# Kernel tuning notes

Hardware: AMD Instinct MI355X
Metric: run time of the kernel (lower is better)

The kernel has to match this reference:

```python
import jax, jax.numpy as jnp
import numpy as np

V = 30000      # user_size / vocab
NINP = 64      # d_word_vec
H = 64         # d_inner_hid
D_NET = 64     # net embedding dim
POS_DIM = 8
NNL1 = 25
NNL2 = 10
MEM = 3
B = 32
LP1 = 101      # seq length before trimming last token


def setup_inputs() -> dict:
    key = jax.random.key(0)
    ks = jax.random.split(key, 16)
    L = LP1 - 1
    u = lambda k, sh: jax.random.uniform(k, sh, jnp.float32, -0.1, 0.1)
    return {
        "encoder_w": u(ks[0], (V, NINP)),
        "pos_w": u(ks[1], (1000, POS_DIM)),
        "w_ih": u(ks[2], (3 * H, NINP + POS_DIM)),
        "w_hh": u(ks[3], (3 * H, H)),
        "b_ih": jnp.zeros((3 * H,), jnp.float32),
        "b_hh": jnp.zeros((3 * H,), jnp.float32),
        "gcn1_w": u(ks[4], (H, H)),
        "gcn1_b": jnp.zeros((H,), jnp.float32),
        "gcn2_w": u(ks[5], (H, D_NET)),
        "gcn2_b": jnp.zeros((H,), jnp.float32),
        "dec_w": u(ks[6], (V, 2 * H)),
        "dec_b": jnp.zeros((V,), jnp.float32),
        "net_emb_tab": jax.random.normal(ks[7], (V, D_NET), jnp.float32),
        "seq": jax.random.randint(ks[8], (B, LP1), 0, V),
        "nb2": jax.random.randint(ks[9], (B * L * NNL1, NNL2), 0, V),
    }


def _forward(encoder_w, pos_w, w_ih, w_hh, b_ih, b_hh,
             gcn1_w, gcn1_b, gcn2_w, gcn2_b, dec_w, dec_b,
             net_emb_tab, seq, nb2):
    inp = seq[:, :-1]                      # (B, L)
    b, L = inp.shape

    # --- GraphSAGE-style 2-hop aggregation (dropout=0, eval mode) ---
    feats = net_emb_tab[nb2]               # (B*L*NNL1, NNL2, D_NET) irregular gather
    nf2 = jax.nn.relu(jnp.mean(feats @ gcn2_w.T + gcn2_b, axis=1))   # (B*L*NNL1, H)
    nf2 = nf2.reshape(b * L, NNL1, H)
    nf1 = jax.nn.relu(jnp.mean(nf2 @ gcn1_w.T + gcn1_b, axis=1))     # (B*L, H)
    nf1 = nf1.reshape(b, L, H)
    # causal memory window of size MEM=3 with zero left-padding, plain mean
    net_pad = jnp.concatenate([jnp.zeros((b, MEM - 1, H), nf1.dtype), nf1], axis=1)
    net_mem = (net_pad[:, 0:L] + net_pad[:, 1:L + 1] + net_pad[:, 2:L + 2]) / MEM  # (B,L,H)

    # --- embeddings + positional ---
    emb = encoder_w[inp]                   # (B, L, NINP)
    pos = jnp.broadcast_to(pos_w[:L][None], (b, L, POS_DIM))
    x = jnp.concatenate([emb, pos], axis=-1)   # (B, L, NINP+POS_DIM)

    # --- GRUCell recurrence via scan (torch gate order: r, z, n) ---
    def gru_step(h, xt):
        gi = xt @ w_ih.T + b_ih            # (B, 3H)
        gh = h @ w_hh.T + b_hh             # (B, 3H)
        i_r, i_z, i_n = jnp.split(gi, 3, axis=-1)
        h_r, h_z, h_n = jnp.split(gh, 3, axis=-1)
        r = jax.nn.sigmoid(i_r + h_r)
        z = jax.nn.sigmoid(i_z + h_z)
        n = jnp.tanh(i_n + r * h_n)
        h_new = (1.0 - z) * n + z * h
        return h_new, h_new

    h0 = jnp.zeros((b, H), x.dtype)
    hidden, hs = jax.lax.scan(gru_step, h0, x.transpose(1, 0, 2))  # hs: (L, B, H)

    outputs = jnp.concatenate([hs.transpose(1, 0, 2), net_mem], axis=-1)  # (B, L, 2H)
    decoded = outputs @ dec_w.T + dec_b    # (B, L, V)

    # --- previous-user scatter mask: -inf at seq[b, :t+1] and at index 0 ---
    tri = jnp.tril(jnp.ones((L, L), bool))
    idx = jnp.where(tri[None], inp[:, None, :], 0)                 # (B, L, L)
    idx = jnp.concatenate([idx, jnp.zeros((b, L, 1), idx.dtype)], axis=-1)
    bidx = jnp.arange(b)[:, None, None]
    tidx = jnp.arange(L)[None, :, None]
    mask = jnp.zeros((b, L, V), decoded.dtype).at[bidx, tidx, idx].set(-jnp.inf)

    result = (decoded + mask).reshape(b * L, V)
    return result, hidden


def reference(encoder_w, pos_w, w_ih, w_hh, b_ih, b_hh,
              gcn1_w, gcn1_b, gcn2_w, gcn2_b, dec_w, dec_b,
              net_emb_tab, seq, nb2):
    return _forward(encoder_w, pos_w, w_ih, w_hh, b_ih, b_hh,
                    gcn1_w, gcn1_b, gcn2_w, gcn2_b, dec_w, dec_b,
                    net_emb_tab, seq, nb2)
```

## Files before the change

### kernel.cpp

```cpp
#include <hip/hip_runtime.h>
#include <math.h>

#define SEQLEN 100
#define BATCH 32
#define HDIM 64
#define VOCAB 30000
#define KDIM 128

#define MASK_NEG (-1.0e30f)

typedef __attribute__((ext_vector_type(8))) short short8;
typedef __attribute__((ext_vector_type(4))) short short4v;
typedef __attribute__((ext_vector_type(4))) float f32x4;

#define WSB_GI     0
#define WSB_NF1    2457600
#define WSB_ABF    3276800
#define WSB_TABBF  4096000
#define WSB_DECWBF 7936000

__device__ __forceinline__ float sigmoidf_(float x) { return 1.0f / (1.0f + expf(-x)); }

__device__ __forceinline__ short f2bf(float f) {
    unsigned u = __builtin_bit_cast(unsigned, f);
    return (short)((u + 0x7fffu + ((u >> 16) & 1u)) >> 16);
}
__device__ __forceinline__ float bf2f(unsigned short s) {
    unsigned u = ((unsigned)s) << 16;
    return __builtin_bit_cast(float, u);
}

__global__ __launch_bounds__(256) void prep_kernel(
    const float* __restrict__ enc, const float* __restrict__ pos_w,
    const float* __restrict__ w_ih, const float* __restrict__ b_ih,
    const int* __restrict__ seq, const float* __restrict__ tab,
    const float* __restrict__ dec_w,
    float* __restrict__ gi, short* __restrict__ tabbf, short* __restrict__ decwbf)
{
    const int tid = threadIdx.x;
    if (blockIdx.x < 100) {
        __shared__ float Wih[192 * 73];
        for (int j = tid; j < 13824; j += 256) {
            int r = j / 72, k = j - r * 72;
            Wih[r * 73 + k] = w_ih[j];
        }
        __syncthreads();
        const int t = blockIdx.x;
        if (tid < 192) {
            const int r = tid;
            const float* wr = &Wih[r * 73];
            const float* pr = pos_w + t * 8;
            float poss = b_ih[r];
            #pragma unroll
            for (int k = 0; k < 8; ++k) poss += pr[k] * wr[64 + k];
            for (int b = 0; b < 32; ++b) {
                const int token = seq[b * 101 + t];
                const float* er = enc + (size_t)token * 64;
                float p0 = 0.f, p1 = 0.f, p2 = 0.f, p3 = 0.f;
                #pragma unroll
                for (int k = 0; k < 64; k += 4) {
                    p0 += er[k + 0] * wr[k + 0];
                    p1 += er[k + 1] * wr[k + 1];
                    p2 += er[k + 2] * wr[k + 2];
                    p3 += er[k + 3] * wr[k + 3];
                }
                gi[(size_t)(t * 32 + b) * 192 + r] = poss + ((p0 + p1) + (p2 + p3));
            }
        }
    } else {
        for (int j = (blockIdx.x - 100) * 256 + tid; j < 1440000; j += 380 * 256) {
            if (j < 480000) {
                float4 v = reinterpret_cast<const float4*>(tab)[j];
                short4v o;
                o[0] = f2bf(v.x); o[1] = f2bf(v.y); o[2] = f2bf(v.z); o[3] = f2bf(v.w);
                *reinterpret_cast<short4v*>(&tabbf[(size_t)j * 4]) = o;
            } else {
                const int k = j - 480000;
                float4 v = reinterpret_cast<const float4*>(dec_w)[k];
                short4v o;
                o[0] = f2bf(v.x); o[1] = f2bf(v.y); o[2] = f2bf(v.z); o[3] = f2bf(v.w);
                *reinterpret_cast<short4v*>(&decwbf[(size_t)k * 4]) = o;
            }
        }
    }
}

union SM {
    struct { float W2t[64][64]; float W1t[64][64]; float sbuf[4][64]; } g;
    struct { float h[64]; float gh[192]; } r;
};
__global__ __launch_bounds__(256) void gcn_gru_kernel(
    const short* __restrict__ tabbf, const int* __restrict__ nb2,
    const float* __restrict__ gcn1_w, const float* __restrict__ gcn1_b,
    const float* __restrict__ gcn2_w, const float* __restrict__ gcn2_b,
    float* __restrict__ nf1,
    const float* __restrict__ gi, const float* __restrict__ w_hh,
    const float* __restrict__ b_hh, short* __restrict__ Abf,
    float* __restrict__ hid_out)
{
    __shared__ SM sm;
    const int tid = threadIdx.x;

    if (blockIdx.x < 32) {
        const int b = blockIdx.x;
        const int r = tid;
        float wreg[64];
        float bh = 0.0f;
        if (r < 192) {
            #pragma unroll
            for (int q = 0; q < 16; ++q) {
                float4 v = *reinterpret_cast<const float4*>(w_hh + r * 64 + q * 4);
                wreg[q * 4 + 0] = v.x; wreg[q * 4 + 1] = v.y;
                wreg[q * 4 + 2] = v.z; wreg[q * 4 + 3] = v.w;
            }
            bh = b_hh[r];
        }
        if (r < 64) sm.r.h[r] = 0.0f;
        __syncthreads();

        for (int t = 0; t < SEQLEN; ++t) {
            if (r < 192) {
                float p0 = bh, p1 = 0.f, p2 = 0.f, p3 = 0.f;
                #pragma unroll
                for (int d = 0; d < 64; d += 4) {
                    const float4 hv = *reinterpret_cast<const float4*>(&sm.r.h[d]);
                    p0 += hv.x * wreg[d + 0];
                    p1 += hv.y * wreg[d + 1];
                    p2 += hv.z * wreg[d + 2];
                    p3 += hv.w * wreg[d + 3];
                }
                sm.r.gh[r] = (p0 + p1) + (p2 + p3);
            }
            __syncthreads();
            if (r < 64) {
                const float* gib = gi + (size_t)(t * 32 + b) * 192;
                float rg = sigmoidf_(gib[r] + sm.r.gh[r]);
                float zg = sigmoidf_(gib[64 + r] + sm.r.gh[64 + r]);
                float ng = tanhf(gib[128 + r] + rg * sm.r.gh[128 + r]);
                float hn = (1.0f - zg) * ng + zg * sm.r.h[r];
                sm.r.h[r] = hn;
                Abf[(size_t)(b * SEQLEN + t) * KDIM + r] = f2bf(hn);
                if (t == SEQLEN - 1) hid_out[b * 64 + r] = hn;
            }
            __syncthreads();
        }
        return;
    }

    for (int idx = tid; idx < 4096; idx += 256) {
        int e = idx >> 6, d = idx & 63;
        sm.g.W2t[d][e] = gcn2_w[idx];
        sm.g.W1t[d][e] = gcn1_w[idx];
    }
    __syncthreads();

    const int wave = tid >> 6;
    const int lane = tid & 63;
    const int p = (blockIdx.x - 32) * 4 + wave;
    const float b2 = gcn2_b[lane];
    const int* __restrict__ nbb = nb2 + (size_t)p * 250;

    float acc = 0.0f;
    for (int i = 0; i < 25; ++i) {
        const int* nb = nbb + i * 10;
        float s0 = 0.f, s1 = 0.f;
        #pragma unroll
        for (int j = 0; j < 10; j += 2) {
            s0 += bf2f((unsigned short)tabbf[(size_t)nb[j] * 64 + lane]);
            s1 += bf2f((unsigned short)tabbf[(size_t)nb[j + 1] * 64 + lane]);
        }
        sm.g.sbuf[wave][lane] = (s0 + s1) * 0.1f;
        __syncthreads();
        float p0 = 0.f, p1 = 0.f, p2 = 0.f, p3 = 0.f;
        #pragma unroll
        for (int d = 0; d < 64; d += 4) {
            p0 += sm.g.sbuf[wave][d + 0] * sm.g.W2t[d + 0][lane];
            p1 += sm.g.sbuf[wave][d + 1] * sm.g.W2t[d + 1][lane];
            p2 += sm.g.sbuf[wave][d + 2] * sm.g.W2t[d + 2][lane];
            p3 += sm.g.sbuf[wave][d + 3] * sm.g.W2t[d + 3][lane];
        }
        acc += fmaxf(((p0 + p1) + (p2 + p3)) + b2, 0.0f);
        __syncthreads();
    }

    sm.g.sbuf[wave][lane] = acc * (1.0f / 25.0f);
    __syncthreads();
    float p0 = 0.f, p1 = 0.f, p2 = 0.f, p3 = 0.f;
    #pragma unroll
    for (int d = 0; d < 64; d += 4) {
        p0 += sm.g.sbuf[wave][d + 0] * sm.g.W1t[d + 0][lane];
        p1 += sm.g.sbuf[wave][d + 1] * sm.g.W1t[d + 1][lane];
        p2 += sm.g.sbuf[wave][d + 2] * sm.g.W1t[d + 2][lane];
        p3 += sm.g.sbuf[wave][d + 3] * sm.g.W1t[d + 3][lane];
    }
    nf1[p * 64 + lane] = fmaxf(((p0 + p1) + (p2 + p3)) + gcn1_b[lane], 0.0f);
}

__global__ __launch_bounds__(256) void netmem_kernel(const float* __restrict__ nf1, short* __restrict__ Abf)
{
    const int idx = blockIdx.x * 256 + threadIdx.x;
    if (idx >= 3200 * 64) return;
    const int p = idx >> 6, e = idx & 63;
    const int t = p % SEQLEN;
    float v = nf1[idx];
    if (t >= 1) v += nf1[idx - 64];
    if (t >= 2) v += nf1[idx - 128];
    Abf[(size_t)p * KDIM + 64 + e] = f2bf(v * (1.0f / 3.0f));
}

#define DN_PANELS 118
#define DM_BLKS   25
#define DNBLK (DM_BLKS * DN_PANELS)
__global__ __launch_bounds__(512) void decode_mfma(
    const short* __restrict__ Abf, const short* __restrict__ Bwbf,
    const float* __restrict__ bias, float* __restrict__ C)
{
    const int lid = blockIdx.x;
    const int q = DNBLK >> 3, r = DNBLK & 7;
    const int xcd = lid & 7, idx = lid >> 3;
    const int swz = (xcd < r ? xcd * (q + 1) : r * (q + 1) + (xcd - r) * q) + idx;
    const int mblk = swz / DN_PANELS;
    const int npanel = swz - mblk * DN_PANELS;

    const int tid = threadIdx.x;
    const int wid = tid >> 6, lane = tid & 63;
    const int lrow = lane & 15;
    const int lkg = lane >> 4;
    const int m0 = mblk * 128 + (wid >> 2) * 64;
    const int n0 = npanel * 256 + (wid & 3) * 64;

    f32x4 acc[4][4];
    #pragma unroll
    for (int mi = 0; mi < 4; ++mi)
        #pragma unroll
        for (int ni = 0; ni < 4; ++ni) acc[mi][ni] = (f32x4)0.0f;

    #pragma unroll
    for (int kc = 0; kc < 4; ++kc) {
        const int kof = kc * 32 + lkg * 8;
        short8 a[4], b[4];
        #pragma unroll
        for (int mi = 0; mi < 4; ++mi)
            a[mi] = *reinterpret_cast<const short8*>(Abf + (size_t)(m0 + mi * 16 + lrow) * KDIM + kof);
        #pragma unroll
        for (int ni = 0; ni < 4; ++ni) {
            const int row = n0 + ni * 16 + lrow;
            b[ni] = (row < VOCAB)
                ? *reinterpret_cast<const short8*>(Bwbf + (size_t)row * KDIM + kof)
                : (short8)0;
        }
        #pragma unroll
        for (int mi = 0; mi < 4; ++mi)
            #pragma unroll
            for (int ni = 0; ni < 4; ++ni)
                acc[mi][ni] = __builtin_amdgcn_mfma_f32_16x16x32_bf16(b[ni], a[mi], acc[mi][ni], 0, 0, 0);
    }

    int colb[4];
    f32x4 bias4[4];
    #pragma unroll
    for (int ni = 0; ni < 4; ++ni) {
        colb[ni] = n0 + ni * 16 + lkg * 4;
        bias4[ni] = (colb[ni] < VOCAB) ? *reinterpret_cast<const f32x4*>(&bias[colb[ni]]) : (f32x4)0.0f;
    }
    #pragma unroll
    for (int mi = 0; mi < 4; ++mi) {
        const size_t rowoff = (size_t)(m0 + mi * 16 + lrow) * VOCAB;
        #pragma unroll
        for (int ni = 0; ni < 4; ++ni) {
            if (colb[ni] < VOCAB)
                *reinterpret_cast<f32x4*>(&C[rowoff + colb[ni]]) = acc[mi][ni] + bias4[ni];
        }
    }
}

__global__ __launch_bounds__(256) void mask_kernel(const int* __restrict__ seq, float* __restrict__ out)
{
    const int w = blockIdx.x * 4 + (threadIdx.x >> 6);
    const int lane = threadIdx.x & 63;
    const int b = w / SEQLEN, t = w % SEQLEN;
    float* row = out + (size_t)w * VOCAB;
    if (lane == 0) row[0] = MASK_NEG;
    for (int j = lane; j <= t; j += 64) row[seq[b * 101 + j]] = MASK_NEG;
}

extern "C" void kernel_launch(void* const* d_in, const int* in_sizes, int n_in,
                              void* d_out, int out_size, void* d_ws, size_t ws_size,
                              hipStream_t stream) {
    const float* encoder_w = (const float*)d_in[0];
    const float* pos_w     = (const float*)d_in[1];
    const float* w_ih      = (const float*)d_in[2];
    const float* w_hh      = (const float*)d_in[3];
    const float* b_ih      = (const float*)d_in[4];
    const float* b_hh      = (const float*)d_in[5];
    const float* gcn1_w    = (const float*)d_in[6];
    const float* gcn1_b    = (const float*)d_in[7];
    const float* gcn2_w    = (const float*)d_in[8];
    const float* gcn2_b    = (const float*)d_in[9];
    const float* dec_w     = (const float*)d_in[10];
    const float* dec_b     = (const float*)d_in[11];
    const float* net_tab   = (const float*)d_in[12];
    const int*   seq       = (const int*)d_in[13];
    const int*   nb2       = (const int*)d_in[14];

    float* out = (float*)d_out;
    float* hid_out = out + (size_t)3200 * VOCAB;

    char* ws = (char*)d_ws;
    float* gi     = (float*)(ws + WSB_GI);
    float* nf1    = (float*)(ws + WSB_NF1);
    short* Abf    = (short*)(ws + WSB_ABF);
    short* tabbf  = (short*)(ws + WSB_TABBF);
    short* decwbf = (short*)(ws + WSB_DECWBF);

    prep_kernel<<<dim3(480), dim3(256), 0, stream>>>(encoder_w, pos_w, w_ih, b_ih, seq, net_tab, dec_w,
                                                     gi, tabbf, decwbf);
    gcn_gru_kernel<<<dim3(832), dim3(256), 0, stream>>>(tabbf, nb2, gcn1_w, gcn1_b, gcn2_w, gcn2_b,
                                                        nf1, gi, w_hh, b_hh, Abf, hid_out);
    netmem_kernel<<<dim3(800), dim3(256), 0, stream>>>(nf1, Abf);
    decode_mfma<<<dim3(DNBLK), dim3(512), 0, stream>>>(Abf, decwbf, dec_b, out);
    mask_kernel<<<dim3(800), dim3(256), 0, stream>>>(seq, out);
}
```

Baseline: 310.1 us.

## Fuse previous-user mask into decode GEMM epilogue and retile to 64-row blocks

```diff
diff --git a/kernel.cpp b/kernel.cpp
--- a/kernel.cpp
+++ b/kernel.cpp
@@ -208,26 +208,34 @@
     Abf[(size_t)p * KDIM + 64 + e] = f2bf(v * (1.0f / 3.0f));
 }
 
+#define DM_BLKS   50
 #define DN_PANELS 118
-#define DM_BLKS   25
 #define DNBLK (DM_BLKS * DN_PANELS)
-__global__ __launch_bounds__(512) void decode_mfma(
+__global__ __launch_bounds__(256, 3) void decode_mfma(
     const short* __restrict__ Abf, const short* __restrict__ Bwbf,
-    const float* __restrict__ bias, float* __restrict__ C)
+    const float* __restrict__ bias, const int* __restrict__ seq,
+    float* __restrict__ C)
 {
     const int lid = blockIdx.x;
     const int q = DNBLK >> 3, r = DNBLK & 7;
     const int xcd = lid & 7, idx = lid >> 3;
     const int swz = (xcd < r ? xcd * (q + 1) : r * (q + 1) + (xcd - r) * q) + idx;
-    const int mblk = swz / DN_PANELS;
-    const int npanel = swz - mblk * DN_PANELS;
+    const int npanel = swz / DM_BLKS;
+    const int mblk = swz - npanel * DM_BLKS;
 
     const int tid = threadIdx.x;
     const int wid = tid >> 6, lane = tid & 63;
     const int lrow = lane & 15;
     const int lkg = lane >> 4;
-    const int m0 = mblk * 128 + (wid >> 2) * 64;
-    const int n0 = npanel * 256 + (wid & 3) * 64;
+    const int m0 = mblk * 64;
+    const int N0 = npanel * 256;
+    const int n0 = N0 + wid * 64;
+
+    __shared__ int seq_l[200];
+    const int b0 = m0 / SEQLEN;
+    const int b1 = (m0 + 63) / SEQLEN;
+    if (tid < 100) seq_l[tid] = seq[b0 * 101 + tid];
+    else if (tid < 200 && b1 != b0) seq_l[tid] = seq[b1 * 101 + (tid - 100)];
 
     f32x4 acc[4][4];
     #pragma unroll
@@ -272,16 +280,20 @@
                 *reinterpret_cast<f32x4*>(&C[rowoff + colb[ni]]) = acc[mi][ni] + bias4[ni];
         }
     }
-}
-
-__global__ __launch_bounds__(256) void mask_kernel(const int* __restrict__ seq, float* __restrict__ out)
-{
-    const int w = blockIdx.x * 4 + (threadIdx.x >> 6);
-    const int lane = threadIdx.x & 63;
-    const int b = w / SEQLEN, t = w % SEQLEN;
-    float* row = out + (size_t)w * VOCAB;
-    if (lane == 0) row[0] = MASK_NEG;
-    for (int j = lane; j <= t; j += 64) row[seq[b * 101 + j]] = MASK_NEG;
+
+    __syncthreads();
+    if (tid < 64) {
+        const int row = m0 + tid;
+        const int b = row / SEQLEN;
+        const int t = row - b * SEQLEN;
+        const int* sl = seq_l + (b - b0) * 100;
+        float* crow = C + (size_t)row * VOCAB;
+        if (N0 == 0) crow[0] = MASK_NEG;
+        for (int j = 0; j <= t; ++j) {
+            const int tok = sl[j];
+            if (tok >= N0 && tok < N0 + 256) crow[tok] = MASK_NEG;
+        }
+    }
 }
 
 extern "C" void kernel_launch(void* const* d_in, const int* in_sizes, int n_in,
@@ -318,6 +330,5 @@
     gcn_gru_kernel<<<dim3(832), dim3(256), 0, stream>>>(tabbf, nb2, gcn1_w, gcn1_b, gcn2_w, gcn2_b,
                                                         nf1, gi, w_hh, b_hh, Abf, hid_out);
     netmem_kernel<<<dim3(800), dim3(256), 0, stream>>>(nf1, Abf);
-    decode_mfma<<<dim3(DNBLK), dim3(512), 0, stream>>>(Abf, decwbf, dec_b, out);
-    mask_kernel<<<dim3(800), dim3(256), 0, stream>>>(seq, out);
-}
+    decode_mfma<<<dim3(DNBLK), dim3(256), 0, stream>>>(Abf, decwbf, dec_b, seq, out);
+}
```

After: 316.9 us. 2.2% more time.

## Fuse kernels: gather fp32 GCN directly, merge netmem into GRU, mask in decode epilogue

Applied to the files above, without the earlier changes.

```diff
diff --git a/kernel.cpp b/kernel.cpp
--- a/kernel.cpp
+++ b/kernel.cpp
@@ -16,8 +16,7 @@
 #define WSB_GI     0
 #define WSB_NF1    2457600
 #define WSB_ABF    3276800
-#define WSB_TABBF  4096000
-#define WSB_DECWBF 7936000
+#define WSB_DECWBF 4096000
 
 __device__ __forceinline__ float sigmoidf_(float x) { return 1.0f / (1.0f + expf(-x)); }
 
@@ -25,30 +24,80 @@
     unsigned u = __builtin_bit_cast(unsigned, f);
     return (short)((u + 0x7fffu + ((u >> 16) & 1u)) >> 16);
 }
-__device__ __forceinline__ float bf2f(unsigned short s) {
-    unsigned u = ((unsigned)s) << 16;
-    return __builtin_bit_cast(float, u);
-}
-
-__global__ __launch_bounds__(256) void prep_kernel(
+
+__global__ __launch_bounds__(256) void prep_gcn_kernel(
+    const float* __restrict__ tab, const int* __restrict__ nb2,
+    const float* __restrict__ gcn1_w, const float* __restrict__ gcn1_b,
+    const float* __restrict__ gcn2_w, const float* __restrict__ gcn2_b,
+    float* __restrict__ nf1,
     const float* __restrict__ enc, const float* __restrict__ pos_w,
     const float* __restrict__ w_ih, const float* __restrict__ b_ih,
-    const int* __restrict__ seq, const float* __restrict__ tab,
-    const float* __restrict__ dec_w,
-    float* __restrict__ gi, short* __restrict__ tabbf, short* __restrict__ decwbf)
+    const int* __restrict__ seq, float* __restrict__ gi,
+    const float* __restrict__ dec_w, short* __restrict__ decwbf)
 {
+    __shared__ struct { float W2t[64][64]; float W1t[64][64]; float sbuf[4][64]; } sm;
     const int tid = threadIdx.x;
-    if (blockIdx.x < 100) {
-        __shared__ float Wih[192 * 73];
-        for (int j = tid; j < 13824; j += 256) {
-            int r = j / 72, k = j - r * 72;
-            Wih[r * 73 + k] = w_ih[j];
+    const int bid = blockIdx.x;
+
+    if (bid < 800) {
+        for (int idx = tid; idx < 4096; idx += 256) {
+            int e = idx >> 6, d = idx & 63;
+            sm.W2t[d][e] = gcn2_w[idx];
+            sm.W1t[d][e] = gcn1_w[idx];
         }
         __syncthreads();
-        const int t = blockIdx.x;
-        if (tid < 192) {
-            const int r = tid;
-            const float* wr = &Wih[r * 73];
+
+        const int wave = tid >> 6;
+        const int lane = tid & 63;
+        const int p = bid * 4 + wave;
+        const float b2 = gcn2_b[lane];
+        const int* __restrict__ nbb = nb2 + (size_t)p * 250;
+
+        float acc = 0.0f;
+        for (int i = 0; i < 25; ++i) {
+            const int* nb = nbb + i * 10;
+            float s0 = 0.f, s1 = 0.f;
+            #pragma unroll
+            for (int j = 0; j < 10; j += 2) {
+                s0 += tab[(size_t)nb[j] * 64 + lane];
+                s1 += tab[(size_t)nb[j + 1] * 64 + lane];
+            }
+            sm.sbuf[wave][lane] = (s0 + s1) * 0.1f;
+            __syncthreads();
+            float p0 = 0.f, p1 = 0.f, p2 = 0.f, p3 = 0.f;
+            #pragma unroll
+            for (int d = 0; d < 64; d += 4) {
+                p0 += sm.sbuf[wave][d + 0] * sm.W2t[d + 0][lane];
+                p1 += sm.sbuf[wave][d + 1] * sm.W2t[d + 1][lane];
+                p2 += sm.sbuf[wave][d + 2] * sm.W2t[d + 2][lane];
+                p3 += sm.sbuf[wave][d + 3] * sm.W2t[d + 3][lane];
+            }
+            acc += fmaxf(((p0 + p1) + (p2 + p3)) + b2, 0.0f);
+            __syncthreads();
+        }
+
+        sm.sbuf[wave][lane] = acc * (1.0f / 25.0f);
+        __syncthreads();
+        float p0 = 0.f, p1 = 0.f, p2 = 0.f, p3 = 0.f;
+        #pragma unroll
+        for (int d = 0; d < 64; d += 4) {
+            p0 += sm.sbuf[wave][d + 0] * sm.W1t[d + 0][lane];
+            p1 += sm.sbuf[wave][d + 1] * sm.W1t[d + 1][lane];
+            p2 += sm.sbuf[wave][d + 2] * sm.W1t[d + 2][lane];
+            p3 += sm.sbuf[wave][d + 3] * sm.W1t[d + 3][lane];
+        }
+        nf1[p * 64 + lane] = fmaxf(((p0 + p1) + (p2 + p3)) + gcn1_b[lane], 0.0f);
+    } else if (bid < 900) {
+        const int t = bid - 800;
+        const int r = tid;
+        if (r < 192) {
+            float wr[72];
+            #pragma unroll
+            for (int q = 0; q < 18; ++q) {
+                float4 v = *reinterpret_cast<const float4*>(w_ih + r * 72 + q * 4);
+                wr[q * 4 + 0] = v.x; wr[q * 4 + 1] = v.y;
+                wr[q * 4 + 2] = v.z; wr[q * 4 + 3] = v.w;
+            }
             const float* pr = pos_w + t * 8;
             float poss = b_ih[r];
             #pragma unroll
@@ -68,37 +117,21 @@
             }
         }
     } else {
-        for (int j = (blockIdx.x - 100) * 256 + tid; j < 1440000; j += 380 * 256) {
-            if (j < 480000) {
-                float4 v = reinterpret_cast<const float4*>(tab)[j];
-                short4v o;
-                o[0] = f2bf(v.x); o[1] = f2bf(v.y); o[2] = f2bf(v.z); o[3] = f2bf(v.w);
-                *reinterpret_cast<short4v*>(&tabbf[(size_t)j * 4]) = o;
-            } else {
-                const int k = j - 480000;
-                float4 v = reinterpret_cast<const float4*>(dec_w)[k];
-                short4v o;
-                o[0] = f2bf(v.x); o[1] = f2bf(v.y); o[2] = f2bf(v.z); o[3] = f2bf(v.w);
-                *reinterpret_cast<short4v*>(&decwbf[(size_t)k * 4]) = o;
-            }
-        }
-    }
-}
-
-union SM {
-    struct { float W2t[64][64]; float W1t[64][64]; float sbuf[4][64]; } g;
-    struct { float h[64]; float gh[192]; } r;
-};
-__global__ __launch_bounds__(256) void gcn_gru_kernel(
-    const short* __restrict__ tabbf, const int* __restrict__ nb2,
-    const float* __restrict__ gcn1_w, const float* __restrict__ gcn1_b,
-    const float* __restrict__ gcn2_w, const float* __restrict__ gcn2_b,
-    float* __restrict__ nf1,
+        for (int j = (bid - 900) * 256 + tid; j < 960000; j += 280 * 256) {
+            float4 v = reinterpret_cast<const float4*>(dec_w)[j];
+            short4v o;
+            o[0] = f2bf(v.x); o[1] = f2bf(v.y); o[2] = f2bf(v.z); o[3] = f2bf(v.w);
+            *reinterpret_cast<short4v*>(&decwbf[(size_t)j * 4]) = o;
+        }
+    }
+}
+
+__global__ __launch_bounds__(256) void gru_netmem_kernel(
     const float* __restrict__ gi, const float* __restrict__ w_hh,
-    const float* __restrict__ b_hh, short* __restrict__ Abf,
-    float* __restrict__ hid_out)
+    const float* __restrict__ b_hh, const float* __restrict__ nf1,
+    short* __restrict__ Abf, float* __restrict__ hid_out)
 {
-    __shared__ SM sm;
+    __shared__ struct { float h[64]; float gh[192]; } sm;
     const int tid = threadIdx.x;
 
     if (blockIdx.x < 32) {
@@ -115,7 +148,7 @@
             }
             bh = b_hh[r];
         }
-        if (r < 64) sm.r.h[r] = 0.0f;
+        if (r < 64) sm.h[r] = 0.0f;
         __syncthreads();
 
         for (int t = 0; t < SEQLEN; ++t) {
@@ -123,22 +156,22 @@
                 float p0 = bh, p1 = 0.f, p2 = 0.f, p3 = 0.f;
                 #pragma unroll
                 for (int d = 0; d < 64; d += 4) {
-                    const float4 hv = *reinterpret_cast<const float4*>(&sm.r.h[d]);
+                    const float4 hv = *reinterpret_cast<const float4*>(&sm.h[d]);
                     p0 += hv.x * wreg[d + 0];
                     p1 += hv.y * wreg[d + 1];
                     p2 += hv.z * wreg[d + 2];
                     p3 += hv.w * wreg[d + 3];
                 }
-                sm.r.gh[r] = (p0 + p1) + (p2 + p3);
+                sm.gh[r] = (p0 + p1) + (p2 + p3);
             }
             __syncthreads();
             if (r < 64) {
                 const float* gib = gi + (size_t)(t * 32 + b) * 192;
-                float rg = sigmoidf_(gib[r] + sm.r.gh[r]);
-                float zg = sigmoidf_(gib[64 + r] + sm.r.gh[64 + r]);
-                float ng = tanhf(gib[128 + r] + rg * sm.r.gh[128 + r]);
-                float hn = (1.0f - zg) * ng + zg * sm.r.h[r];
-                sm.r.h[r] = hn;
+                float rg = sigmoidf_(gib[r] + sm.gh[r]);
+                float zg = sigmoidf_(gib[64 + r] + sm.gh[64 + r]);
+                float ng = tanhf(gib[128 + r] + rg * sm.gh[128 + r]);
+                float hn = (1.0f - zg) * ng + zg * sm.h[r];
+                sm.h[r] = hn;
                 Abf[(size_t)(b * SEQLEN + t) * KDIM + r] = f2bf(hn);
                 if (t == SEQLEN - 1) hid_out[b * 64 + r] = hn;
             }
@@ -147,59 +180,7 @@
         return;
     }
 
-    for (int idx = tid; idx < 4096; idx += 256) {
-        int e = idx >> 6, d = idx & 63;
-        sm.g.W2t[d][e] = gcn2_w[idx];
-        sm.g.W1t[d][e] = gcn1_w[idx];
-    }
-    __syncthreads();
-
-    const int wave = tid >> 6;
-    const int lane = tid & 63;
-    const int p = (blockIdx.x - 32) * 4 + wave;
-    const float b2 = gcn2_b[lane];
-    const int* __restrict__ nbb = nb2 + (size_t)p * 250;
-
-    float acc = 0.0f;
-    for (int i = 0; i < 25; ++i) {
-        const int* nb = nbb + i * 10;
-        float s0 = 0.f, s1 = 0.f;
-        #pragma unroll
-        for (int j = 0; j < 10; j += 2) {
-            s0 += bf2f((unsigned short)tabbf[(size_t)nb[j] * 64 + lane]);
-            s1 += bf2f((unsigned short)tabbf[(size_t)nb[j + 1] * 64 + lane]);
-        }
-        sm.g.sbuf[wave][lane] = (s0 + s1) * 0.1f;
-        __syncthreads();
-        float p0 = 0.f, p1 = 0.f, p2 = 0.f, p3 = 0.f;
-        #pragma unroll
-        for (int d = 0; d < 64; d += 4) {
-            p0 += sm.g.sbuf[wave][d + 0] * sm.g.W2t[d + 0][lane];
-            p1 += sm.g.sbuf[wave][d + 1] * sm.g.W2t[d + 1][lane];
-            p2 += sm.g.sbuf[wave][d + 2] * sm.g.W2t[d + 2][lane];
-            p3 += sm.g.sbuf[wave][d + 3] * sm.g.W2t[d + 3][lane];
-        }
-        acc += fmaxf(((p0 + p1) + (p2 + p3)) + b2, 0.0f);
-        __syncthreads();
-    }
-
-    sm.g.sbuf[wave][lane] = acc * (1.0f / 25.0f);
-    __syncthreads();
-    float p0 = 0.f, p1 = 0.f, p2 = 0.f, p3 = 0.f;
-    #pragma unroll
-    for (int d = 0; d < 64; d += 4) {
-        p0 += sm.g.sbuf[wave][d + 0] * sm.g.W1t[d + 0][lane];
-        p1 += sm.g.sbuf[wave][d + 1] * sm.g.W1t[d + 1][lane];
-        p2 += sm.g.sbuf[wave][d + 2] * sm.g.W1t[d + 2][lane];
-        p3 += sm.g.sbuf[wave][d + 3] * sm.g.W1t[d + 3][lane];
-    }
-    nf1[p * 64 + lane] = fmaxf(((p0 + p1) + (p2 + p3)) + gcn1_b[lane], 0.0f);
-}
-
-__global__ __launch_bounds__(256) void netmem_kernel(const float* __restrict__ nf1, short* __restrict__ Abf)
-{
-    const int idx = blockIdx.x * 256 + threadIdx.x;
-    if (idx >= 3200 * 64) return;
+    const int idx = (blockIdx.x - 32) * 256 + tid;
     const int p = idx >> 6, e = idx & 63;
     const int t = p % SEQLEN;
     float v = nf1[idx];
@@ -213,7 +194,8 @@
 #define DNBLK (DM_BLKS * DN_PANELS)
 __global__ __launch_bounds__(512) void decode_mfma(
     const short* __restrict__ Abf, const short* __restrict__ Bwbf,
-    const float* __restrict__ bias, float* __restrict__ C)
+    const float* __restrict__ bias, const int* __restrict__ seq,
+    float* __restrict__ C)
 {
     const int lid = blockIdx.x;
     const int q = DNBLK >> 3, r = DNBLK & 7;
@@ -226,8 +208,18 @@
     const int wid = tid >> 6, lane = tid & 63;
     const int lrow = lane & 15;
     const int lkg = lane >> 4;
-    const int m0 = mblk * 128 + (wid >> 2) * 64;
-    const int n0 = npanel * 256 + (wid & 3) * 64;
+    const int M0 = mblk * 128;
+    const int N0 = npanel * 256;
+    const int m0 = M0 + (wid >> 2) * 64;
+    const int n0 = N0 + (wid & 3) * 64;
+
+    __shared__ int seq_l[300];
+    const int b_lo = M0 / SEQLEN;
+    const int nbt = (M0 + 127) / SEQLEN - b_lo + 1;
+    if (tid < nbt * 100) {
+        const int bb = b_lo + tid / 100;
+        if (bb < 32) seq_l[tid] = seq[bb * 101 + (tid % 100)];
+    }
 
     f32x4 acc[4][4];
     #pragma unroll
@@ -272,16 +264,20 @@
                 *reinterpret_cast<f32x4*>(&C[rowoff + colb[ni]]) = acc[mi][ni] + bias4[ni];
         }
     }
-}
-
-__global__ __launch_bounds__(256) void mask_kernel(const int* __restrict__ seq, float* __restrict__ out)
-{
-    const int w = blockIdx.x * 4 + (threadIdx.x >> 6);
-    const int lane = threadIdx.x & 63;
-    const int b = w / SEQLEN, t = w % SEQLEN;
-    float* row = out + (size_t)w * VOCAB;
-    if (lane == 0) row[0] = MASK_NEG;
-    for (int j = lane; j <= t; j += 64) row[seq[b * 101 + j]] = MASK_NEG;
+
+    __syncthreads();
+    if (tid < 128) {
+        const int row = M0 + tid;
+        const int b = row / SEQLEN;
+        const int t = row - b * SEQLEN;
+        const int* sl = seq_l + (b - b_lo) * 100;
+        float* crow = C + (size_t)row * VOCAB;
+        if (npanel == 0) crow[0] = MASK_NEG;
+        for (int j = 0; j <= t; ++j) {
+            const unsigned tok = (unsigned)(sl[j] - N0);
+            if (tok < 256u) crow[N0 + (int)tok] = MASK_NEG;
+        }
+    }
 }
 
 extern "C" void kernel_launch(void* const* d_in, const int* in_sizes, int n_in,
@@ -310,14 +306,11 @@
     float* gi     = (float*)(ws + WSB_GI);
     float* nf1    = (float*)(ws + WSB_NF1);
     short* Abf    = (short*)(ws + WSB_ABF);
-    short* tabbf  = (short*)(ws + WSB_TABBF);
     short* decwbf = (short*)(ws + WSB_DECWBF);
 
-    prep_kernel<<<dim3(480), dim3(256), 0, stream>>>(encoder_w, pos_w, w_ih, b_ih, seq, net_tab, dec_w,
-                                                     gi, tabbf, decwbf);
-    gcn_gru_kernel<<<dim3(832), dim3(256), 0, stream>>>(tabbf, nb2, gcn1_w, gcn1_b, gcn2_w, gcn2_b,
-                                                        nf1, gi, w_hh, b_hh, Abf, hid_out);
-    netmem_kernel<<<dim3(800), dim3(256), 0, stream>>>(nf1, Abf);
-    decode_mfma<<<dim3(DNBLK), dim3(512), 0, stream>>>(Abf, decwbf, dec_b, out);
-    mask_kernel<<<dim3(800), dim3(256), 0, stream>>>(seq, out);
-}
+    prep_gcn_kernel<<<dim3(1180), dim3(256), 0, stream>>>(
+        net_tab, nb2, gcn1_w, gcn1_b, gcn2_w, gcn2_b, nf1,
+        encoder_w, pos_w, w_ih, b_ih, seq, gi, dec_w, decwbf);
+    gru_netmem_kernel<<<dim3(832), dim3(256), 0, stream>>>(gi, w_hh, b_hh, nf1, Abf, hid_out);
+    decode_mfma<<<dim3(DNBLK), dim3(512), 0, stream>>>(Abf, decwbf, dec_b, seq, out);
+}
```

New measurement: 342.4 us. 10.4% more time.

## Fuse mask scatter into decoder epilogue and prefetch GRU input gates

Applied to the files above, without the earlier changes.

```diff
diff --git a/kernel.cpp b/kernel.cpp
--- a/kernel.cpp
+++ b/kernel.cpp
@@ -39,16 +39,16 @@
 {
     const int tid = threadIdx.x;
     if (blockIdx.x < 100) {
-        __shared__ float Wih[192 * 73];
-        for (int j = tid; j < 13824; j += 256) {
-            int r = j / 72, k = j - r * 72;
-            Wih[r * 73 + k] = w_ih[j];
-        }
-        __syncthreads();
         const int t = blockIdx.x;
-        if (tid < 192) {
-            const int r = tid;
-            const float* wr = &Wih[r * 73];
+        const int r = tid;
+        if (r < 192) {
+            float wr[72];
+            #pragma unroll
+            for (int q = 0; q < 18; ++q) {
+                float4 v = *reinterpret_cast<const float4*>(w_ih + r * 72 + q * 4);
+                wr[q * 4 + 0] = v.x; wr[q * 4 + 1] = v.y;
+                wr[q * 4 + 2] = v.z; wr[q * 4 + 3] = v.w;
+            }
             const float* pr = pos_w + t * 8;
             float poss = b_ih[r];
             #pragma unroll
@@ -59,10 +59,11 @@
                 float p0 = 0.f, p1 = 0.f, p2 = 0.f, p3 = 0.f;
                 #pragma unroll
                 for (int k = 0; k < 64; k += 4) {
-                    p0 += er[k + 0] * wr[k + 0];
-                    p1 += er[k + 1] * wr[k + 1];
-                    p2 += er[k + 2] * wr[k + 2];
-                    p3 += er[k + 3] * wr[k + 3];
+                    const float4 ev = *reinterpret_cast<const float4*>(er + k);
+                    p0 += ev.x * wr[k + 0];
+                    p1 += ev.y * wr[k + 1];
+                    p2 += ev.z * wr[k + 2];
+                    p3 += ev.w * wr[k + 3];
                 }
                 gi[(size_t)(t * 32 + b) * 192 + r] = poss + ((p0 + p1) + (p2 + p3));
             }
@@ -87,7 +88,7 @@
 
 union SM {
     struct { float W2t[64][64]; float W1t[64][64]; float sbuf[4][64]; } g;
-    struct { float h[64]; float gh[192]; } r;
+    struct { float h[64]; float gh[192]; float gn[64]; } r;
 };
 __global__ __launch_bounds__(256) void gcn_gru_kernel(
     const short* __restrict__ tabbf, const int* __restrict__ nb2,
@@ -102,6 +103,7 @@
     const int tid = threadIdx.x;
 
     if (blockIdx.x < 32) {
+        __builtin_amdgcn_s_setprio(1);
         const int b = blockIdx.x;
         const int r = tid;
         float wreg[64];
@@ -115,10 +117,15 @@
             }
             bh = b_hh[r];
         }
+        float h_own = 0.0f;
         if (r < 64) sm.r.h[r] = 0.0f;
+        float gv = (r < 192) ? gi[(size_t)b * 192 + r] : 0.0f;
         __syncthreads();
 
         for (int t = 0; t < SEQLEN; ++t) {
+            float gvn = gv;
+            if (r < 192 && t < SEQLEN - 1)
+                gvn = gi[(size_t)((t + 1) * 32 + b) * 192 + r];
             if (r < 192) {
                 float p0 = bh, p1 = 0.f, p2 = 0.f, p3 = 0.f;
                 #pragma unroll
@@ -129,19 +136,26 @@
                     p2 += hv.z * wreg[d + 2];
                     p3 += hv.w * wreg[d + 3];
                 }
-                sm.r.gh[r] = (p0 + p1) + (p2 + p3);
+                const float dot = (p0 + p1) + (p2 + p3);
+                if (r < 128) {
+                    sm.r.gh[r] = gv + dot;
+                } else {
+                    sm.r.gh[r] = dot;
+                    sm.r.gn[r - 128] = gv;
+                }
             }
             __syncthreads();
             if (r < 64) {
-                const float* gib = gi + (size_t)(t * 32 + b) * 192;
-                float rg = sigmoidf_(gib[r] + sm.r.gh[r]);
-                float zg = sigmoidf_(gib[64 + r] + sm.r.gh[64 + r]);
-                float ng = tanhf(gib[128 + r] + rg * sm.r.gh[128 + r]);
-                float hn = (1.0f - zg) * ng + zg * sm.r.h[r];
+                const float rg = sigmoidf_(sm.r.gh[r]);
+                const float zg = sigmoidf_(sm.r.gh[64 + r]);
+                const float ng = tanhf(sm.r.gn[r] + rg * sm.r.gh[128 + r]);
+                const float hn = (1.0f - zg) * ng + zg * h_own;
+                h_own = hn;
                 sm.r.h[r] = hn;
                 Abf[(size_t)(b * SEQLEN + t) * KDIM + r] = f2bf(hn);
                 if (t == SEQLEN - 1) hid_out[b * 64 + r] = hn;
             }
+            gv = gvn;
             __syncthreads();
         }
         return;
@@ -213,7 +227,8 @@
 #define DNBLK (DM_BLKS * DN_PANELS)
 __global__ __launch_bounds__(512) void decode_mfma(
     const short* __restrict__ Abf, const short* __restrict__ Bwbf,
-    const float* __restrict__ bias, float* __restrict__ C)
+    const float* __restrict__ bias, const int* __restrict__ seq,
+    float* __restrict__ C)
 {
     const int lid = blockIdx.x;
     const int q = DNBLK >> 3, r = DNBLK & 7;
@@ -226,8 +241,18 @@
     const int wid = tid >> 6, lane = tid & 63;
     const int lrow = lane & 15;
     const int lkg = lane >> 4;
-    const int m0 = mblk * 128 + (wid >> 2) * 64;
-    const int n0 = npanel * 256 + (wid & 3) * 64;
+    const int M0 = mblk * 128;
+    const int N0 = npanel * 256;
+    const int m0 = M0 + (wid >> 2) * 64;
+    const int n0 = N0 + (wid & 3) * 64;
+
+    __shared__ int seq_l[300];
+    const int b_lo = M0 / SEQLEN;
+    const int nbt = (M0 + 127) / SEQLEN - b_lo + 1;
+    if (tid < nbt * 100) {
+        const int bb = b_lo + tid / 100;
+        if (bb < 32) seq_l[tid] = seq[bb * 101 + (tid % 100)];
+    }
 
     f32x4 acc[4][4];
     #pragma unroll
@@ -272,16 +297,20 @@
                 *reinterpret_cast<f32x4*>(&C[rowoff + colb[ni]]) = acc[mi][ni] + bias4[ni];
         }
     }
-}
-
-__global__ __launch_bounds__(256) void mask_kernel(const int* __restrict__ seq, float* __restrict__ out)
-{
-    const int w = blockIdx.x * 4 + (threadIdx.x >> 6);
-    const int lane = threadIdx.x & 63;
-    const int b = w / SEQLEN, t = w % SEQLEN;
-    float* row = out + (size_t)w * VOCAB;
-    if (lane == 0) row[0] = MASK_NEG;
-    for (int j = lane; j <= t; j += 64) row[seq[b * 101 + j]] = MASK_NEG;
+
+    __syncthreads();
+    if (tid < 128) {
+        const int row = M0 + tid;
+        const int b = row / SEQLEN;
+        const int t = row - b * SEQLEN;
+        const int* sl = seq_l + (b - b_lo) * 100;
+        float* crow = C + (size_t)row * VOCAB;
+        if (npanel == 0) crow[0] = MASK_NEG;
+        for (int j = 0; j <= t; ++j) {
+            const unsigned tok = (unsigned)(sl[j] - N0);
+            if (tok < 256u) crow[N0 + (int)tok] = MASK_NEG;
+        }
+    }
 }
 
 extern "C" void kernel_launch(void* const* d_in, const int* in_sizes, int n_in,
@@ -318,6 +347,5 @@
     gcn_gru_kernel<<<dim3(832), dim3(256), 0, stream>>>(tabbf, nb2, gcn1_w, gcn1_b, gcn2_w, gcn2_b,
                                                         nf1, gi, w_hh, b_hh, Abf, hid_out);
     netmem_kernel<<<dim3(800), dim3(256), 0, stream>>>(nf1, Abf);
-    decode_mfma<<<dim3(DNBLK), dim3(512), 0, stream>>>(Abf, decwbf, dec_b, out);
-    mask_kernel<<<dim3(800), dim3(256), 0, stream>>>(seq, out);
-}
+    decode_mfma<<<dim3(DNBLK), dim3(512), 0, stream>>>(Abf, decwbf, dec_b, seq, out);
+}
```

Measured after the change: 287.0 us. 1.08x faster.
